# Optimization experiments

Measured on AMD Instinct MI355X. Metric: run time of the kernel, lower is better.

The kernel has to match this reference:

```python
import jax, jax.numpy as jnp
import numpy as np
from jax.ops import segment_sum

NUM_HEADS = 16
NEG_INF = -jnp.inf


def setup_inputs() -> dict:
    key = jax.random.key(0)
    ks = jax.random.split(key, 12)
    D, H = 1024, NUM_HEADS
    SRC, TGT = 2048, 2048
    V, EV = 32000, 2000
    s = 1.0 / np.sqrt(D)
    return {
        "logits": jax.random.normal(ks[0], (TGT, V), jnp.float32),
        "extended_vocab_ids": jax.random.randint(ks[1], (SRC,), 0, V + EV, jnp.int32),
        "src_subtokens": jax.random.normal(ks[2], (SRC, D), jnp.float32),
        "tgt_subtokens": jax.random.normal(ks[3], (TGT, D), jnp.float32),
        "w_q": jax.random.normal(ks[4], (D, D), jnp.float32) * s,
        "b_q": jax.random.normal(ks[5], (D,), jnp.float32) * 0.02,
        "w_k": jax.random.normal(ks[6], (D, D), jnp.float32) * s,
        "b_k": jax.random.normal(ks[7], (D,), jnp.float32) * 0.02,
        "w_ptr": jax.random.normal(ks[8], (D,), jnp.float32) * s,
        "b_ptr": jax.random.normal(ks[9], (1,), jnp.float32) * 0.02,
        "len_vocab": V,
        "len_extended_vocab": EV,
    }


def _mha_attention(query, key, w_q, b_q, w_k, b_k):
    # SimpleMHA.unbatched_forward: project q/k, per-head scaled dot-product
    # softmax over src, mean over heads -> [TGT, SRC]
    TGT, D = query.shape
    SRC = key.shape[0]
    hd = D // NUM_HEADS
    q = (query @ w_q.T + b_q).reshape(TGT, NUM_HEADS, hd)
    k = (key @ w_k.T + b_k).reshape(SRC, NUM_HEADS, hd)
    scores = jnp.einsum("thd,shd->hts", q, k) / jnp.sqrt(jnp.float32(hd))
    attn = jax.nn.softmax(scores, axis=-1)  # [H, TGT, SRC]
    return attn.mean(axis=0)  # [TGT, SRC]


def reference(logits, extended_vocab_ids, src_subtokens, tgt_subtokens,
              w_q, b_q, w_k, b_k, w_ptr, b_ptr, len_vocab, len_extended_vocab):
    total = len_vocab + len_extended_vocab
    eps = jnp.finfo(jnp.float32).eps
    fmin = jnp.finfo(jnp.float32).min

    # copy gate: sigmoid(Linear(tgt)) -> [TGT, 1]
    copy_prob = jax.nn.sigmoid(tgt_subtokens @ w_ptr + b_ptr[0])[:, None]

    # attention distribution over src tokens [TGT, SRC]
    attn = _mha_attention(tgt_subtokens, src_subtokens, w_q, b_q, w_k, b_k)

    # attention @ one-hot(M) == scatter-add of attention columns by vocab id
    attn_vocab = segment_sum(attn.T, extended_vocab_ids, num_segments=total).T  # [TGT, total]
    attn_vocab = jnp.where(attn_vocab == 0, eps, attn_vocab)
    pointer_log_probs = jnp.log(attn_vocab)

    decoder_log_probs = jax.nn.log_softmax(logits, axis=1)
    decoder_log_probs = jnp.pad(decoder_log_probs, ((0, 0), (0, len_extended_vocab)),
                                constant_values=NEG_INF)

    p = jnp.stack([decoder_log_probs + jnp.log(1.0 - copy_prob),
                   pointer_log_probs + jnp.log(copy_prob)])
    p = jnp.where(p == NEG_INF, fmin, p)
    return jax.scipy.special.logsumexp(p, axis=0)
```

## Files before the change

kernel.cpp:

```cpp
#include <hip/hip_runtime.h>

typedef __attribute__((ext_vector_type(8))) short short8;
typedef __attribute__((ext_vector_type(4))) float f32x4;
typedef __attribute__((ext_vector_type(4))) unsigned int u32x4;
typedef unsigned short u16;
typedef unsigned int u32;

#define MFMA16 __builtin_amdgcn_mfma_f32_16x16x32_bf16

static constexpr int TGT = 2048, SRCN = 2048, DIM = 1024, NH = 16;
static constexpr int NV = 32000, NTOT = 34000;
#define FLT_EPS 1.1920928955078125e-07f

__device__ __forceinline__ u16 f2bf(float f) {
  unsigned u = __float_as_uint(f);
  return (u16)((u + 0x7FFFu + ((u >> 16) & 1u)) >> 16);
}

__device__ __forceinline__ int swz8(int row, int seg) {
  return row * 64 + ((seg ^ (row & 7)) << 3);
}

__global__ __launch_bounds__(256) void proj_gemm(
    const float* __restrict__ Xq, const float* __restrict__ Wq,
    const float* __restrict__ Bq, u16* __restrict__ Cq,
    const float* __restrict__ Xk, const float* __restrict__ Wk,
    const float* __restrict__ Bk, u16* __restrict__ Ck) {
  const int zz = blockIdx.z;
  const float* X = zz ? Xk : Xq;
  const float* W = zz ? Wk : Wq;
  const float* bias = zz ? Bk : Bq;
  u16* C = zz ? Ck : Cq;
  const float scale = zz ? 1.0f : 0.125f;

  __shared__ u16 As[128 * 32];
  __shared__ u16 Bs[128 * 32];
  const int n0 = blockIdx.x * 128, m0 = blockIdx.y * 128;
  const int tid = threadIdx.x, lane = tid & 63, w = tid >> 6;
  const int wr = w >> 1, wc = w & 1;
  const int srow = tid >> 1, shalf = tid & 1;
  f32x4 acc[4][4] = {};

  for (int k0 = 0; k0 < DIM; k0 += 32) {
    __syncthreads();
    {
      const float* pa = X + (size_t)(m0 + srow) * DIM + k0 + shalf * 16;
      const float* pb = W + (size_t)(n0 + srow) * DIM + k0 + shalf * 16;
      float4 a0 = ((const float4*)pa)[0], a1 = ((const float4*)pa)[1];
      float4 a2 = ((const float4*)pa)[2], a3 = ((const float4*)pa)[3];
      float4 b0 = ((const float4*)pb)[0], b1 = ((const float4*)pb)[1];
      float4 b2 = ((const float4*)pb)[2], b3 = ((const float4*)pb)[3];
      short8 wa0, wa1, wb0, wb1;
      wa0[0]=(short)f2bf(a0.x); wa0[1]=(short)f2bf(a0.y); wa0[2]=(short)f2bf(a0.z); wa0[3]=(short)f2bf(a0.w);
      wa0[4]=(short)f2bf(a1.x); wa0[5]=(short)f2bf(a1.y); wa0[6]=(short)f2bf(a1.z); wa0[7]=(short)f2bf(a1.w);
      wa1[0]=(short)f2bf(a2.x); wa1[1]=(short)f2bf(a2.y); wa1[2]=(short)f2bf(a2.z); wa1[3]=(short)f2bf(a2.w);
      wa1[4]=(short)f2bf(a3.x); wa1[5]=(short)f2bf(a3.y); wa1[6]=(short)f2bf(a3.z); wa1[7]=(short)f2bf(a3.w);
      wb0[0]=(short)f2bf(b0.x); wb0[1]=(short)f2bf(b0.y); wb0[2]=(short)f2bf(b0.z); wb0[3]=(short)f2bf(b0.w);
      wb0[4]=(short)f2bf(b1.x); wb0[5]=(short)f2bf(b1.y); wb0[6]=(short)f2bf(b1.z); wb0[7]=(short)f2bf(b1.w);
      wb1[0]=(short)f2bf(b2.x); wb1[1]=(short)f2bf(b2.y); wb1[2]=(short)f2bf(b2.z); wb1[3]=(short)f2bf(b2.w);
      wb1[4]=(short)f2bf(b3.x); wb1[5]=(short)f2bf(b3.y); wb1[6]=(short)f2bf(b3.z); wb1[7]=(short)f2bf(b3.w);
      int swz = (srow >> 1) & 3;
      int sg0 = ((shalf * 2 + 0) ^ swz) << 3;
      int sg1 = ((shalf * 2 + 1) ^ swz) << 3;
      *(short8*)&As[srow * 32 + sg0] = wa0;
      *(short8*)&As[srow * 32 + sg1] = wa1;
      *(short8*)&Bs[srow * 32 + sg0] = wb0;
      *(short8*)&Bs[srow * 32 + sg1] = wb1;
    }
    __syncthreads();
    const int kq = lane >> 4;
    short8 af[4], bfr[4];
    for (int f = 0; f < 4; ++f) {
      int ar = wr * 64 + f * 16 + (lane & 15);
      af[f] = *(const short8*)&As[ar * 32 + ((kq ^ ((ar >> 1) & 3)) << 3)];
      int br = wc * 64 + f * 16 + (lane & 15);
      bfr[f] = *(const short8*)&Bs[br * 32 + ((kq ^ ((br >> 1) & 3)) << 3)];
    }
    for (int fr = 0; fr < 4; ++fr)
      for (int fc = 0; fc < 4; ++fc)
        acc[fr][fc] = MFMA16(af[fr], bfr[fc], acc[fr][fc], 0, 0, 0);
  }

  for (int fc = 0; fc < 4; ++fc) {
    int col = n0 + wc * 64 + fc * 16 + (lane & 15);
    float bv = bias[col];
    for (int fr = 0; fr < 4; ++fr)
      for (int r = 0; r < 4; ++r) {
        int rowm = m0 + wr * 64 + fr * 16 + ((lane >> 4) << 2) + r;
        C[(size_t)rowm * DIM + col] = f2bf((acc[fr][fc][r] + bv) * scale);
      }
  }
}

__global__ __launch_bounds__(256) void zsum_kernel(const u16* __restrict__ Qb,
                                                   const u16* __restrict__ Kb,
                                                   float* __restrict__ Zinv) {
  __shared__ u16 Ks[64 * 64];
  const int h = blockIdx.x, t0 = blockIdx.y * 64;
  const int tid = threadIdx.x, lane = tid & 63, w = tid >> 6;
  const int arow = t0 + w * 16 + (lane & 15);
  const int acol = h * 64 + ((lane >> 4) << 3);
  short8 a0 = *(const short8*)&Qb[(size_t)arow * DIM + acol];
  short8 a1 = *(const short8*)&Qb[(size_t)arow * DIM + acol + 32];
  float zacc[4] = {0.f, 0.f, 0.f, 0.f};

  for (int s0 = 0; s0 < SRCN; s0 += 64) {
    __syncthreads();
    for (int q = tid; q < 512; q += 256) {
      int r = q >> 3, seg = q & 7;
      *(short8*)&Ks[swz8(r, seg)] = *(const short8*)&Kb[(size_t)(s0 + r) * DIM + h * 64 + seg * 8];
    }
    __syncthreads();
    for (int sub = 0; sub < 4; ++sub) {
      int brow = sub * 16 + (lane & 15);
      int slo = (lane >> 4);
      short8 b0 = *(const short8*)&Ks[swz8(brow, slo)];
      short8 b1 = *(const short8*)&Ks[swz8(brow, slo + 4)];
      f32x4 c = {0.f, 0.f, 0.f, 0.f};
      c = MFMA16(a0, b0, c, 0, 0, 0);
      c = MFMA16(a1, b1, c, 0, 0, 0);
      zacc[0] += __expf(c[0]); zacc[1] += __expf(c[1]);
      zacc[2] += __expf(c[2]); zacc[3] += __expf(c[3]);
    }
  }
  for (int d = 1; d < 16; d <<= 1) {
    zacc[0] += __shfl_xor(zacc[0], d, 64);
    zacc[1] += __shfl_xor(zacc[1], d, 64);
    zacc[2] += __shfl_xor(zacc[2], d, 64);
    zacc[3] += __shfl_xor(zacc[3], d, 64);
  }
  if ((lane & 15) == 0) {
    int trow = t0 + w * 16 + ((lane >> 4) << 2);
    for (int r = 0; r < 4; ++r)
      Zinv[h * TGT + trow + r] = 1.0f / (16.0f * zacc[r]);
  }
}

__global__ __launch_bounds__(256) void fused_mid_kernel(
    const u16* __restrict__ Qb, const u16* __restrict__ Kb,
    const float* __restrict__ Zinv, float* __restrict__ attn,
    const float* __restrict__ logits, const float* __restrict__ tgt,
    const float* __restrict__ w_ptr, const float* __restrict__ b_ptr,
    const int* __restrict__ ids, int* __restrict__ sperm,
    u32* __restrict__ segmap, float4* __restrict__ rowc) {
  __shared__ __align__(16) char smem[20480];
  const int b = blockIdx.x;
  const int tid = threadIdx.x, lane = tid & 63, w = tid >> 6;

  if (b == 0) {
    int* kk_ = (int*)smem;
    int* vv_ = (int*)(smem + 8192);
    for (int i = tid; i < 2048; i += 256) { kk_[i] = ids[i]; vv_[i] = i; }
    __syncthreads();
    for (int kk = 2; kk <= 2048; kk <<= 1)
      for (int j = kk >> 1; j > 0; j >>= 1) {
        for (int m = tid; m < 1024; m += 256) {
          int i = ((m & ~(j - 1)) << 1) | (m & (j - 1));
          int l = i | j;
          bool asc = ((i & kk) == 0);
          int ki = kk_[i], kl = kk_[l];
          if ((ki > kl) == asc) {
            kk_[i] = kl; kk_[l] = ki;
            int tv = vv_[i]; vv_[i] = vv_[l]; vv_[l] = tv;
          }
        }
        __syncthreads();
      }
    for (int i = tid; i < 2048; i += 256) sperm[i] = vv_[i];
    for (int i = tid; i < NTOT; i += 256) segmap[i] = 0xFFFFFFFFu;
    __syncthreads();
    for (int p = tid; p < 2048; p += 256) {
      int id = kk_[p];
      if (p > 0 && kk_[p - 1] == id) continue;
      int q = p + 1;
      while (q < 2048 && kk_[q] == id) ++q;
      segmap[id] = (u32)p | ((u32)(q - p) << 16);
    }
    return;
  }

  if (b <= 1024) {
    u16* Qs = (u16*)smem;
    u16* Ks = (u16*)(smem + 8192);
    float* izs = (float*)(smem + 16384);
    const int bb = b - 1;
    const int s0 = (bb & 31) * 64, t0 = (bb >> 5) * 64;
    const int wr = w >> 1, wc = w & 1;
    for (int q = tid; q < 1024; q += 256) izs[q] = Zinv[(q >> 6) * TGT + t0 + (q & 63)];
    f32x4 acc[2][2] = {};

    for (int h = 0; h < NH; ++h) {
      __syncthreads();
      for (int q = tid; q < 512; q += 256) {
        int r = q >> 3, seg = q & 7;
        *(short8*)&Qs[swz8(r, seg)] = *(const short8*)&Qb[(size_t)(t0 + r) * DIM + h * 64 + seg * 8];
        *(short8*)&Ks[swz8(r, seg)] = *(const short8*)&Kb[(size_t)(s0 + r) * DIM + h * 64 + seg * 8];
      }
      __syncthreads();
      f32x4 sc[2][2] = {};
      for (int kk = 0; kk < 2; ++kk) {
        int seg = (lane >> 4) + kk * 4;
        short8 a0 = *(const short8*)&Qs[swz8(wr * 32 + (lane & 15), seg)];
        short8 a1 = *(const short8*)&Qs[swz8(wr * 32 + 16 + (lane & 15), seg)];
        short8 b0 = *(const short8*)&Ks[swz8(wc * 32 + (lane & 15), seg)];
        short8 b1 = *(const short8*)&Ks[swz8(wc * 32 + 16 + (lane & 15), seg)];
        sc[0][0] = MFMA16(a0, b0, sc[0][0], 0, 0, 0);
        sc[0][1] = MFMA16(a0, b1, sc[0][1], 0, 0, 0);
        sc[1][0] = MFMA16(a1, b0, sc[1][0], 0, 0, 0);
        sc[1][1] = MFMA16(a1, b1, sc[1][1], 0, 0, 0);
      }
      for (int fr = 0; fr < 2; ++fr)
        for (int fc = 0; fc < 2; ++fc)
          for (int r = 0; r < 4; ++r) {
            float iz = izs[h * 64 + wr * 32 + fr * 16 + ((lane >> 4) << 2) + r];
            acc[fr][fc][r] += __expf(sc[fr][fc][r]) * iz;
          }
    }
    for (int fr = 0; fr < 2; ++fr)
      for (int fc = 0; fc < 2; ++fc)
        for (int r = 0; r < 4; ++r) {
          int t = t0 + wr * 32 + fr * 16 + ((lane >> 4) << 2) + r;
          int s = s0 + wc * 32 + fc * 16 + (lane & 15);
          attn[(size_t)t * SRCN + s] = acc[fr][fc][r];
        }
    return;
  }

  float* red = (float*)smem;
  const int t = b - 1025;
  const f32x4* l4 = (const f32x4*)(logits + (size_t)t * NV);
  float e0 = 0.f, e1 = 0.f, e2 = 0.f, e3 = 0.f;
  const f32x4 z4 = {0.f, 0.f, 0.f, 0.f};
#pragma unroll 2
  for (int pk = 0; pk < 8; ++pk) {
    int g0 = pk * 1024 + tid;
    int g1 = g0 + 256, g2 = g0 + 512, g3 = g0 + 768;
    bool d0 = g0 < NV / 4, d1 = g1 < NV / 4, d2 = g2 < NV / 4, d3 = g3 < NV / 4;
    f32x4 v0 = d0 ? l4[g0] : z4;
    f32x4 v1 = d1 ? l4[g1] : z4;
    f32x4 v2 = d2 ? l4[g2] : z4;
    f32x4 v3 = d3 ? l4[g3] : z4;
    float s0 = (__expf(v0.x) + __expf(v0.y)) + (__expf(v0.z) + __expf(v0.w));
    float s1 = (__expf(v1.x) + __expf(v1.y)) + (__expf(v1.z) + __expf(v1.w));
    float s2 = (__expf(v2.x) + __expf(v2.y)) + (__expf(v2.z) + __expf(v2.w));
    float s3 = (__expf(v3.x) + __expf(v3.y)) + (__expf(v3.z) + __expf(v3.w));
    e0 += d0 ? s0 : 0.f;
    e1 += d1 ? s1 : 0.f;
    e2 += d2 ? s2 : 0.f;
    e3 += d3 ? s3 : 0.f;
  }
  float es = (e0 + e1) + (e2 + e3);

  float4 xv = *(const float4*)&tgt[(size_t)t * DIM + tid * 4];
  float4 wv = *(const float4*)&w_ptr[tid * 4];
  float g = (xv.x * wv.x + xv.y * wv.y) + (xv.z * wv.z + xv.w * wv.w);
  for (int d = 1; d < 64; d <<= 1) {
    es += __shfl_xor(es, d, 64);
    g += __shfl_xor(g, d, 64);
  }
  if (lane == 0) { red[w] = es; red[4 + w] = g; }
  __syncthreads();
  if (tid == 0) {
    float tot = red[0] + red[1] + red[2] + red[3];
    float gs = red[4] + red[5] + red[6] + red[7] + b_ptr[0];
    float c = 1.0f / (1.0f + __expf(-gs));
    float4 rc;
    rc.x = (1.0f - c) / tot;
    rc.y = c * FLT_EPS;
    rc.z = c;
    rc.w = 0.f;
    rowc[t] = rc;
  }
}

__global__ __launch_bounds__(512) void out_kernel(
    const float* __restrict__ logits, const float4* __restrict__ rowc,
    const int* __restrict__ sperm, const u32* __restrict__ segmap,
    const float* __restrict__ attn, float* __restrict__ out) {
  const int t = blockIdx.x;
  const int tid = threadIdx.x;
  float4 rc = rowc[t];
  const float K1 = rc.x, Ceps = rc.y, cc = rc.z;
  const f32x4* l4 = (const f32x4*)(logits + (size_t)t * NV);
  const float* arow = attn + (size_t)t * SRCN;
  f32x4* o4 = (f32x4*)(out + (size_t)t * NTOT);
  const u32x4* m4 = (const u32x4*)segmap;

  auto psum = [&](u32 mv) -> float {
    if (mv == 0xFFFFFFFFu) return Ceps;
    int p = (int)(mv & 0xFFFFu), n = (int)(mv >> 16);
    float s = 0.f;
    for (int q = 0; q < n; ++q) s += arow[sperm[p + q]];
    return cc * s;
  };
  auto elem = [&](float v, bool d, u32 mv) -> float {
    float e = d ? __expf(v) : 0.f;
    return __logf(fmaf(e, K1, psum(mv)));
  };

  const f32x4 z4 = {0.f, 0.f, 0.f, 0.f};
#pragma unroll
  for (int pk = 0; pk < 4; ++pk) {
    int g0 = pk * 2048 + tid;
    int g1 = g0 + 512, g2 = g0 + 1024, g3 = g0 + 1536;
    u32x4 m0 = m4[g0], m1 = m4[g1], m2 = m4[g2], m3 = m4[g3];
    bool d0 = g0 < NV / 4, d1 = g1 < NV / 4, d2 = g2 < NV / 4, d3 = g3 < NV / 4;
    f32x4 v0 = d0 ? __builtin_nontemporal_load(&l4[g0]) : z4;
    f32x4 v1 = d1 ? __builtin_nontemporal_load(&l4[g1]) : z4;
    f32x4 v2 = d2 ? __builtin_nontemporal_load(&l4[g2]) : z4;
    f32x4 v3 = d3 ? __builtin_nontemporal_load(&l4[g3]) : z4;
    f32x4 o0, o1, o2, o3;
    o0.x = elem(v0.x, d0, m0.x); o0.y = elem(v0.y, d0, m0.y);
    o0.z = elem(v0.z, d0, m0.z); o0.w = elem(v0.w, d0, m0.w);
    o1.x = elem(v1.x, d1, m1.x); o1.y = elem(v1.y, d1, m1.y);
    o1.z = elem(v1.z, d1, m1.z); o1.w = elem(v1.w, d1, m1.w);
    o2.x = elem(v2.x, d2, m2.x); o2.y = elem(v2.y, d2, m2.y);
    o2.z = elem(v2.z, d2, m2.z); o2.w = elem(v2.w, d2, m2.w);
    o3.x = elem(v3.x, d3, m3.x); o3.y = elem(v3.y, d3, m3.y);
    o3.z = elem(v3.z, d3, m3.z); o3.w = elem(v3.w, d3, m3.w);
    __builtin_nontemporal_store(o0, &o4[g0]);
    __builtin_nontemporal_store(o1, &o4[g1]);
    __builtin_nontemporal_store(o2, &o4[g2]);
    __builtin_nontemporal_store(o3, &o4[g3]);
  }
  for (int g = 8192 + tid; g < NTOT / 4; g += 512) {
    u32x4 m = m4[g];
    f32x4 o;
    o.x = __logf(psum(m.x));
    o.y = __logf(psum(m.y));
    o.z = __logf(psum(m.z));
    o.w = __logf(psum(m.w));
    __builtin_nontemporal_store(o, &o4[g]);
  }
}

extern "C" void kernel_launch(void* const* d_in, const int* in_sizes, int n_in,
                              void* d_out, int out_size, void* d_ws, size_t ws_size,
                              hipStream_t stream) {
  const float* logits = (const float*)d_in[0];
  const int* ids      = (const int*)d_in[1];
  const float* src    = (const float*)d_in[2];
  const float* tgt    = (const float*)d_in[3];
  const float* w_q    = (const float*)d_in[4];
  const float* b_q    = (const float*)d_in[5];
  const float* w_k    = (const float*)d_in[6];
  const float* b_k    = (const float*)d_in[7];
  const float* w_ptr  = (const float*)d_in[8];
  const float* b_ptr  = (const float*)d_in[9];
  float* out = (float*)d_out;

  char* ws = (char*)d_ws;
  u16* Qb     = (u16*)(ws);
  u16* Kb     = (u16*)(ws + (size_t)4 * 1024 * 1024);
  float* Zinv = (float*)(ws + (size_t)8 * 1024 * 1024);
  float* attn = (float*)(ws + (size_t)8 * 1024 * 1024 + 131072);
  char* tail  = ws + (size_t)8 * 1024 * 1024 + 131072 + (size_t)16 * 1024 * 1024;
  int* sperm  = (int*)(tail);
  u32* segmap = (u32*)(tail + 8192);
  float4* rowc = (float4*)(tail + 8192 + 136000);

  proj_gemm<<<dim3(8, 16, 2), 256, 0, stream>>>(tgt, w_q, b_q, Qb, src, w_k, b_k, Kb);
  zsum_kernel<<<dim3(16, 32), 256, 0, stream>>>(Qb, Kb, Zinv);
  fused_mid_kernel<<<3073, 256, 0, stream>>>(Qb, Kb, Zinv, attn, logits, tgt,
                                             w_ptr, b_ptr, ids, sperm, segmap, rowc);
  out_kernel<<<TGT, 512, 0, stream>>>(logits, rowc, sperm, segmap, attn, out);
}
```

Measured before the change: 275.0 us.

## Precompute per-segment pointer sums in LDS via compacted unique-id list

```diff
diff --git a/kernel.cpp b/kernel.cpp
--- a/kernel.cpp
+++ b/kernel.cpp
@@ -19,6 +19,109 @@
 
 __device__ __forceinline__ int swz8(int row, int seg) {
   return row * 64 + ((seg ^ (row & 7)) << 3);
+}
+
+__device__ __forceinline__ void stats_row_body(
+    int t, const float* __restrict__ logits, const float* __restrict__ tgt,
+    const float* __restrict__ w_ptr, const float* __restrict__ b_ptr,
+    float4* __restrict__ rowc, int tid, int lane, int w, float* red) {
+  const f32x4* l4 = (const f32x4*)(logits + (size_t)t * NV);
+  float e0 = 0.f, e1 = 0.f, e2 = 0.f, e3 = 0.f;
+  const f32x4 z4 = {0.f, 0.f, 0.f, 0.f};
+#pragma unroll 2
+  for (int pk = 0; pk < 8; ++pk) {
+    int g0 = pk * 1024 + tid;
+    int g1 = g0 + 256, g2 = g0 + 512, g3 = g0 + 768;
+    bool d0 = g0 < NV / 4, d1 = g1 < NV / 4, d2 = g2 < NV / 4, d3 = g3 < NV / 4;
+    f32x4 v0 = d0 ? l4[g0] : z4;
+    f32x4 v1 = d1 ? l4[g1] : z4;
+    f32x4 v2 = d2 ? l4[g2] : z4;
+    f32x4 v3 = d3 ? l4[g3] : z4;
+    float s0 = (__expf(v0.x) + __expf(v0.y)) + (__expf(v0.z) + __expf(v0.w));
+    float s1 = (__expf(v1.x) + __expf(v1.y)) + (__expf(v1.z) + __expf(v1.w));
+    float s2 = (__expf(v2.x) + __expf(v2.y)) + (__expf(v2.z) + __expf(v2.w));
+    float s3 = (__expf(v3.x) + __expf(v3.y)) + (__expf(v3.z) + __expf(v3.w));
+    e0 += d0 ? s0 : 0.f;
+    e1 += d1 ? s1 : 0.f;
+    e2 += d2 ? s2 : 0.f;
+    e3 += d3 ? s3 : 0.f;
+  }
+  float es = (e0 + e1) + (e2 + e3);
+
+  float4 xv = *(const float4*)&tgt[(size_t)t * DIM + tid * 4];
+  float4 wv = *(const float4*)&w_ptr[tid * 4];
+  float g = (xv.x * wv.x + xv.y * wv.y) + (xv.z * wv.z + xv.w * wv.w);
+  for (int d = 1; d < 64; d <<= 1) {
+    es += __shfl_xor(es, d, 64);
+    g += __shfl_xor(g, d, 64);
+  }
+  if (lane == 0) { red[w] = es; red[4 + w] = g; }
+  __syncthreads();
+  if (tid == 0) {
+    float tot = red[0] + red[1] + red[2] + red[3];
+    float gs = red[4] + red[5] + red[6] + red[7] + b_ptr[0];
+    float c = 1.0f / (1.0f + __expf(-gs));
+    float4 rc;
+    rc.x = (1.0f - c) / tot;
+    rc.y = c * FLT_EPS;
+    rc.z = c;
+    rc.w = 0.f;
+    rowc[t] = rc;
+  }
+}
+
+__device__ __forceinline__ void sort_body(
+    const int* __restrict__ ids, int* __restrict__ sperm,
+    u32* __restrict__ segmap, u32* __restrict__ ustart,
+    int tid, int lane, int w, char* smem) {
+  int* kk_ = (int*)smem;
+  int* vv_ = (int*)(smem + 8192);
+  int* scan = (int*)(smem + 16384);
+  for (int i = tid; i < 2048; i += 256) { kk_[i] = ids[i]; vv_[i] = i; }
+  for (int i = tid; i < 2048; i += 256) ustart[i] = 0xFFFFFFFFu;
+  if (tid == 0) scan[4] = 0;
+  __syncthreads();
+  for (int kk = 2; kk <= 2048; kk <<= 1)
+    for (int j = kk >> 1; j > 0; j >>= 1) {
+      for (int m = tid; m < 1024; m += 256) {
+        int i = ((m & ~(j - 1)) << 1) | (m & (j - 1));
+        int l = i | j;
+        bool asc = ((i & kk) == 0);
+        int ki = kk_[i], kl = kk_[l];
+        if ((ki > kl) == asc) {
+          kk_[i] = kl; kk_[l] = ki;
+          int tv = vv_[i]; vv_[i] = vv_[l]; vv_[l] = tv;
+        }
+      }
+      __syncthreads();
+    }
+  for (int i = tid; i < 2048; i += 256) sperm[i] = vv_[i];
+  for (int i = tid; i < NTOT; i += 256) segmap[i] = 0xFFFFFFFFu;
+  __syncthreads();
+  for (int c = 0; c < 8; ++c) {
+    int p = c * 256 + tid;
+    int id = kk_[p];
+    bool head = (p == 0) || (kk_[p - 1] != id);
+    unsigned long long bal = __ballot(head);
+    int lanepfx = __popcll(bal & ((1ull << lane) - 1ull));
+    int wtot = __popcll(bal);
+    if (lane == 0) scan[w] = wtot;
+    __syncthreads();
+    int woff = 0;
+    for (int i = 0; i < w; ++i) woff += scan[i];
+    int base = scan[4];
+    if (head) {
+      int q = p + 1;
+      while (q < 2048 && kk_[q] == id) ++q;
+      int rank = base + woff + lanepfx;
+      u32 cnt = (u32)(q - p);
+      segmap[id] = (u32)rank | (cnt << 16);
+      ustart[rank] = (u32)p | (cnt << 16);
+    }
+    __syncthreads();
+    if (tid == 0) scan[4] = base + scan[0] + scan[1] + scan[2] + scan[3];
+    __syncthreads();
+  }
 }
 
 __global__ __launch_bounds__(256) void proj_gemm(
@@ -142,156 +245,96 @@
     const float* __restrict__ logits, const float* __restrict__ tgt,
     const float* __restrict__ w_ptr, const float* __restrict__ b_ptr,
     const int* __restrict__ ids, int* __restrict__ sperm,
-    u32* __restrict__ segmap, float4* __restrict__ rowc) {
+    u32* __restrict__ segmap, u32* __restrict__ ustart,
+    float4* __restrict__ rowc) {
   __shared__ __align__(16) char smem[20480];
   const int b = blockIdx.x;
   const int tid = threadIdx.x, lane = tid & 63, w = tid >> 6;
 
   if (b == 0) {
-    int* kk_ = (int*)smem;
-    int* vv_ = (int*)(smem + 8192);
-    for (int i = tid; i < 2048; i += 256) { kk_[i] = ids[i]; vv_[i] = i; }
-    __syncthreads();
-    for (int kk = 2; kk <= 2048; kk <<= 1)
-      for (int j = kk >> 1; j > 0; j >>= 1) {
-        for (int m = tid; m < 1024; m += 256) {
-          int i = ((m & ~(j - 1)) << 1) | (m & (j - 1));
-          int l = i | j;
-          bool asc = ((i & kk) == 0);
-          int ki = kk_[i], kl = kk_[l];
-          if ((ki > kl) == asc) {
-            kk_[i] = kl; kk_[l] = ki;
-            int tv = vv_[i]; vv_[i] = vv_[l]; vv_[l] = tv;
-          }
-        }
-        __syncthreads();
+    sort_body(ids, sperm, segmap, ustart, tid, lane, w, smem);
+    return;
+  }
+  if (b > 1024) {
+    stats_row_body(b - 1025, logits, tgt, w_ptr, b_ptr, rowc,
+                   tid, lane, w, (float*)smem);
+    return;
+  }
+  u16* Qs = (u16*)smem;
+  u16* Ks = (u16*)(smem + 8192);
+  const int bb = b - 1;
+  const int s0 = (bb & 31) * 64, t0 = (bb >> 5) * 64;
+  const int wr = w >> 1, wc = w & 1;
+  f32x4 acc[2][2] = {};
+
+  for (int h = 0; h < NH; ++h) {
+    __syncthreads();
+    for (int q = tid; q < 512; q += 256) {
+      int r = q >> 3, seg = q & 7;
+      *(short8*)&Qs[swz8(r, seg)] = *(const short8*)&Qb[(size_t)(t0 + r) * DIM + h * 64 + seg * 8];
+      *(short8*)&Ks[swz8(r, seg)] = *(const short8*)&Kb[(size_t)(s0 + r) * DIM + h * 64 + seg * 8];
+    }
+    __syncthreads();
+    f32x4 sc[2][2] = {};
+    for (int kk = 0; kk < 2; ++kk) {
+      int seg = (lane >> 4) + kk * 4;
+      short8 a0 = *(const short8*)&Qs[swz8(wr * 32 + (lane & 15), seg)];
+      short8 a1 = *(const short8*)&Qs[swz8(wr * 32 + 16 + (lane & 15), seg)];
+      short8 b0 = *(const short8*)&Ks[swz8(wc * 32 + (lane & 15), seg)];
+      short8 b1 = *(const short8*)&Ks[swz8(wc * 32 + 16 + (lane & 15), seg)];
+      sc[0][0] = MFMA16(a0, b0, sc[0][0], 0, 0, 0);
+      sc[0][1] = MFMA16(a0, b1, sc[0][1], 0, 0, 0);
+      sc[1][0] = MFMA16(a1, b0, sc[1][0], 0, 0, 0);
+      sc[1][1] = MFMA16(a1, b1, sc[1][1], 0, 0, 0);
+    }
+    for (int fr = 0; fr < 2; ++fr) {
+      int trow = t0 + wr * 32 + fr * 16 + ((lane >> 4) << 2);
+      float4 z4 = *(const float4*)&Zinv[h * TGT + trow];
+      float iz[4] = {z4.x, z4.y, z4.z, z4.w};
+      for (int fc = 0; fc < 2; ++fc)
+        for (int r = 0; r < 4; ++r)
+          acc[fr][fc][r] += __expf(sc[fr][fc][r]) * iz[r];
+    }
+  }
+  for (int fr = 0; fr < 2; ++fr)
+    for (int fc = 0; fc < 2; ++fc)
+      for (int r = 0; r < 4; ++r) {
+        int t = t0 + wr * 32 + fr * 16 + ((lane >> 4) << 2) + r;
+        int s = s0 + wc * 32 + fc * 16 + (lane & 15);
+        attn[(size_t)t * SRCN + s] = acc[fr][fc][r];
       }
-    for (int i = tid; i < 2048; i += 256) sperm[i] = vv_[i];
-    for (int i = tid; i < NTOT; i += 256) segmap[i] = 0xFFFFFFFFu;
-    __syncthreads();
-    for (int p = tid; p < 2048; p += 256) {
-      int id = kk_[p];
-      if (p > 0 && kk_[p - 1] == id) continue;
-      int q = p + 1;
-      while (q < 2048 && kk_[q] == id) ++q;
-      segmap[id] = (u32)p | ((u32)(q - p) << 16);
-    }
-    return;
-  }
-
-  if (b <= 1024) {
-    u16* Qs = (u16*)smem;
-    u16* Ks = (u16*)(smem + 8192);
-    float* izs = (float*)(smem + 16384);
-    const int bb = b - 1;
-    const int s0 = (bb & 31) * 64, t0 = (bb >> 5) * 64;
-    const int wr = w >> 1, wc = w & 1;
-    for (int q = tid; q < 1024; q += 256) izs[q] = Zinv[(q >> 6) * TGT + t0 + (q & 63)];
-    f32x4 acc[2][2] = {};
-
-    for (int h = 0; h < NH; ++h) {
-      __syncthreads();
-      for (int q = tid; q < 512; q += 256) {
-        int r = q >> 3, seg = q & 7;
-        *(short8*)&Qs[swz8(r, seg)] = *(const short8*)&Qb[(size_t)(t0 + r) * DIM + h * 64 + seg * 8];
-        *(short8*)&Ks[swz8(r, seg)] = *(const short8*)&Kb[(size_t)(s0 + r) * DIM + h * 64 + seg * 8];
-      }
-      __syncthreads();
-      f32x4 sc[2][2] = {};
-      for (int kk = 0; kk < 2; ++kk) {
-        int seg = (lane >> 4) + kk * 4;
-        short8 a0 = *(const short8*)&Qs[swz8(wr * 32 + (lane & 15), seg)];
-        short8 a1 = *(const short8*)&Qs[swz8(wr * 32 + 16 + (lane & 15), seg)];
-        short8 b0 = *(const short8*)&Ks[swz8(wc * 32 + (lane & 15), seg)];
-        short8 b1 = *(const short8*)&Ks[swz8(wc * 32 + 16 + (lane & 15), seg)];
-        sc[0][0] = MFMA16(a0, b0, sc[0][0], 0, 0, 0);
-        sc[0][1] = MFMA16(a0, b1, sc[0][1], 0, 0, 0);
-        sc[1][0] = MFMA16(a1, b0, sc[1][0], 0, 0, 0);
-        sc[1][1] = MFMA16(a1, b1, sc[1][1], 0, 0, 0);
-      }
-      for (int fr = 0; fr < 2; ++fr)
-        for (int fc = 0; fc < 2; ++fc)
-          for (int r = 0; r < 4; ++r) {
-            float iz = izs[h * 64 + wr * 32 + fr * 16 + ((lane >> 4) << 2) + r];
-            acc[fr][fc][r] += __expf(sc[fr][fc][r]) * iz;
-          }
-    }
-    for (int fr = 0; fr < 2; ++fr)
-      for (int fc = 0; fc < 2; ++fc)
-        for (int r = 0; r < 4; ++r) {
-          int t = t0 + wr * 32 + fr * 16 + ((lane >> 4) << 2) + r;
-          int s = s0 + wc * 32 + fc * 16 + (lane & 15);
-          attn[(size_t)t * SRCN + s] = acc[fr][fc][r];
-        }
-    return;
-  }
-
-  float* red = (float*)smem;
-  const int t = b - 1025;
-  const f32x4* l4 = (const f32x4*)(logits + (size_t)t * NV);
-  float e0 = 0.f, e1 = 0.f, e2 = 0.f, e3 = 0.f;
-  const f32x4 z4 = {0.f, 0.f, 0.f, 0.f};
-#pragma unroll 2
-  for (int pk = 0; pk < 8; ++pk) {
-    int g0 = pk * 1024 + tid;
-    int g1 = g0 + 256, g2 = g0 + 512, g3 = g0 + 768;
-    bool d0 = g0 < NV / 4, d1 = g1 < NV / 4, d2 = g2 < NV / 4, d3 = g3 < NV / 4;
-    f32x4 v0 = d0 ? l4[g0] : z4;
-    f32x4 v1 = d1 ? l4[g1] : z4;
-    f32x4 v2 = d2 ? l4[g2] : z4;
-    f32x4 v3 = d3 ? l4[g3] : z4;
-    float s0 = (__expf(v0.x) + __expf(v0.y)) + (__expf(v0.z) + __expf(v0.w));
-    float s1 = (__expf(v1.x) + __expf(v1.y)) + (__expf(v1.z) + __expf(v1.w));
-    float s2 = (__expf(v2.x) + __expf(v2.y)) + (__expf(v2.z) + __expf(v2.w));
-    float s3 = (__expf(v3.x) + __expf(v3.y)) + (__expf(v3.z) + __expf(v3.w));
-    e0 += d0 ? s0 : 0.f;
-    e1 += d1 ? s1 : 0.f;
-    e2 += d2 ? s2 : 0.f;
-    e3 += d3 ? s3 : 0.f;
-  }
-  float es = (e0 + e1) + (e2 + e3);
-
-  float4 xv = *(const float4*)&tgt[(size_t)t * DIM + tid * 4];
-  float4 wv = *(const float4*)&w_ptr[tid * 4];
-  float g = (xv.x * wv.x + xv.y * wv.y) + (xv.z * wv.z + xv.w * wv.w);
-  for (int d = 1; d < 64; d <<= 1) {
-    es += __shfl_xor(es, d, 64);
-    g += __shfl_xor(g, d, 64);
-  }
-  if (lane == 0) { red[w] = es; red[4 + w] = g; }
-  __syncthreads();
-  if (tid == 0) {
-    float tot = red[0] + red[1] + red[2] + red[3];
-    float gs = red[4] + red[5] + red[6] + red[7] + b_ptr[0];
-    float c = 1.0f / (1.0f + __expf(-gs));
-    float4 rc;
-    rc.x = (1.0f - c) / tot;
-    rc.y = c * FLT_EPS;
-    rc.z = c;
-    rc.w = 0.f;
-    rowc[t] = rc;
-  }
 }
 
 __global__ __launch_bounds__(512) void out_kernel(
     const float* __restrict__ logits, const float4* __restrict__ rowc,
     const int* __restrict__ sperm, const u32* __restrict__ segmap,
-    const float* __restrict__ attn, float* __restrict__ out) {
-  const int t = blockIdx.x;
+    const u32* __restrict__ ustart, const float* __restrict__ attn,
+    float* __restrict__ out) {
+  __shared__ float aL[2048];
+  __shared__ float pL[2048];
+  const int t = (TGT - 1) - blockIdx.x;
   const int tid = threadIdx.x;
   float4 rc = rowc[t];
   const float K1 = rc.x, Ceps = rc.y, cc = rc.z;
   const f32x4* l4 = (const f32x4*)(logits + (size_t)t * NV);
-  const float* arow = attn + (size_t)t * SRCN;
   f32x4* o4 = (f32x4*)(out + (size_t)t * NTOT);
   const u32x4* m4 = (const u32x4*)segmap;
 
+  *(float4*)&aL[tid * 4] = *(const float4*)&attn[(size_t)t * SRCN + tid * 4];
+  __syncthreads();
+  for (int r = tid; r < 2048; r += 512) {
+    u32 u = ustart[r];
+    if (u != 0xFFFFFFFFu) {
+      int p = (int)(u & 0xFFFFu), n = (int)(u >> 16);
+      float s = 0.f;
+      for (int k = 0; k < n; ++k) s += aL[sperm[p + k]];
+      pL[r] = cc * s;
+    }
+  }
+  __syncthreads();
+
   auto psum = [&](u32 mv) -> float {
-    if (mv == 0xFFFFFFFFu) return Ceps;
-    int p = (int)(mv & 0xFFFFu), n = (int)(mv >> 16);
-    float s = 0.f;
-    for (int q = 0; q < n; ++q) s += arow[sperm[p + q]];
-    return cc * s;
+    return (mv == 0xFFFFFFFFu) ? Ceps : pL[mv & 0xFFFFu];
   };
   auto elem = [&](float v, bool d, u32 mv) -> float {
     float e = d ? __expf(v) : 0.f;
@@ -354,14 +397,16 @@
   u16* Kb     = (u16*)(ws + (size_t)4 * 1024 * 1024);
   float* Zinv = (float*)(ws + (size_t)8 * 1024 * 1024);
   float* attn = (float*)(ws + (size_t)8 * 1024 * 1024 + 131072);
-  char* tail  = ws + (size_t)8 * 1024 * 1024 + 131072 + (size_t)16 * 1024 * 1024;
-  int* sperm  = (int*)(tail);
-  u32* segmap = (u32*)(tail + 8192);
-  float4* rowc = (float4*)(tail + 8192 + 136000);
+  size_t tail_off = (size_t)8 * 1024 * 1024 + 131072 + (size_t)16 * 1024 * 1024;
+  int* sperm   = (int*)(ws + tail_off);
+  u32* segmap  = (u32*)(ws + tail_off + 8192);
+  u32* ustart  = (u32*)(ws + tail_off + 8192 + 136000);
+  float4* rowc = (float4*)(ws + tail_off + 8192 + 136000 + 8192);
 
   proj_gemm<<<dim3(8, 16, 2), 256, 0, stream>>>(tgt, w_q, b_q, Qb, src, w_k, b_k, Kb);
   zsum_kernel<<<dim3(16, 32), 256, 0, stream>>>(Qb, Kb, Zinv);
   fused_mid_kernel<<<3073, 256, 0, stream>>>(Qb, Kb, Zinv, attn, logits, tgt,
-                                             w_ptr, b_ptr, ids, sperm, segmap, rowc);
-  out_kernel<<<TGT, 512, 0, stream>>>(logits, rowc, sperm, segmap, attn, out);
-}
+                                             w_ptr, b_ptr, ids, sperm, segmap,
+                                             ustart, rowc);
+  out_kernel<<<TGT, 512, 0, stream>>>(logits, rowc, sperm, segmap, ustart, attn, out);
+}
```

Result: faster. 245.7 us (-10.6%).
